# Kernel optimization log

Hardware: AMD Instinct MI355X
Metric: run time of the kernel (lower is better)

## Reference

```python
import jax, jax.numpy as jnp
import numpy as np

B = 8192
N_CLASSES = 10

_AX = 'abcd'
_CNOT = jnp.array([[1, 0, 0, 0], [0, 1, 0, 0], [0, 0, 0, 1], [0, 0, 1, 0]], jnp.float32).reshape(2, 2, 2, 2)


def _ry(theta):
    c, s = jnp.cos(theta / 2), jnp.sin(theta / 2)
    return jnp.stack([jnp.stack([c, -s]), jnp.stack([s, c])])  # [2,2]


def _ap1(state, U, w):
    # apply single-qubit gate U on wire w; state: [N,2,2,2,2]
    i = _AX[:w] + 'i' + _AX[w + 1:]
    o = _AX[:w] + 'o' + _AX[w + 1:]
    return jnp.einsum(f'oi,n{i}->n{o}', U, state)


def _ap2(state, U, w0, w1):
    # apply two-qubit gate U [2,2,2,2]=(out0,out1,in0,in1) on wires (w0,w1)
    i, o = list(_AX), list(_AX)
    i[w0], i[w1] = 'i', 'j'
    o[w0], o[w1] = 'o', 'p'
    return jnp.einsum(f"opij,n{''.join(i)}->n{''.join(o)}", U, state)


def quantum_features(data, q_params):
    # data: [N,4] RY encoding angles applied to |0000>
    h = data / 2
    v = jnp.stack([jnp.cos(h), jnp.sin(h)], -1)  # [N,4,2]
    state = jnp.einsum('na,nb,nc,nd->nabcd', v[:, 0], v[:, 1], v[:, 2], v[:, 3])
    # fixed 8-op random layer instance (real-valued): 5 RY + 3 CNOT
    state = _ap1(state, _ry(q_params[0]), 0)
    state = _ap1(state, _ry(q_params[1]), 1)
    state = _ap2(state, _CNOT, 0, 1)
    state = _ap1(state, _ry(q_params[2]), 2)
    state = _ap1(state, _ry(q_params[3]), 3)
    state = _ap2(state, _CNOT, 2, 3)
    state = _ap1(state, _ry(q_params[4]), 1)
    state = _ap2(state, _CNOT, 1, 2)
    probs = state * state  # real statevector -> |amp|^2
    sgn = jnp.array([1.0, -1.0], jnp.float32)
    z = jnp.stack([
        jnp.einsum('nabcd,a->n', probs, sgn),
        jnp.einsum('nabcd,b->n', probs, sgn),
        jnp.einsum('nabcd,c->n', probs, sgn),
        jnp.einsum('nabcd,d->n', probs, sgn)], -1)
    return z  # [N,4] PauliZ expectations


def setup_inputs() -> dict:
    key = jax.random.key(0)
    ks = jax.random.split(key, 6)
    return {
        'x': jax.random.normal(ks[0], (B, 1, 28, 28), jnp.float32),
        'conv_w': jax.random.normal(ks[1], (4, 1, 2, 2), jnp.float32) * 0.5,
        'conv_b': jax.random.normal(ks[2], (4,), jnp.float32) * 0.1,
        'q_params': jax.random.uniform(ks[3], (5,), jnp.float32, 0.0, 2.0 * np.pi),
        'lin_w': jax.random.normal(ks[4], (N_CLASSES, 1568), jnp.float32) * 0.02,
        'lin_b': jnp.zeros((N_CLASSES,), jnp.float32),
    }


def reference(x, conv_w, conv_b, q_params, lin_w, lin_b):
    feats = jax.lax.conv_general_dilated(
        x, conv_w, window_strides=(2, 2), padding='VALID',
        dimension_numbers=('NCHW', 'OIHW', 'NCHW')) + conv_b[None, :, None, None]
    bsz = feats.shape[0]
    flat = feats.reshape(bsz, -1)  # [B,784]
    # extractor views flat as [B,28,28] and takes 2x2 patches -> [B*196,4]
    patches = flat.reshape(bsz, 14, 2, 14, 2).transpose(0, 1, 3, 2, 4).reshape(bsz * 196, 4)
    q = quantum_features(patches, q_params).reshape(bsz, 784)
    combined = jnp.concatenate([flat, q], axis=1)  # [B,1568]
    logits = combined @ lin_w.T + lin_b
    return jax.nn.log_softmax(logits, axis=-1)
```

## Files before the change

### kernel.cpp

```cpp
#include <hip/hip_runtime.h>
#include <hip/hip_bf16.h>


#define SPB 8
#define THREADS 256
#define NCLS 10
#define FEAT 1568

__global__ __launch_bounds__(THREADS, 3)
void quanv_fused_kernel(const float* __restrict__ x,
                        const float* __restrict__ conv_w,
                        const float* __restrict__ conv_b,
                        const float* __restrict__ q_params,
                        const float* __restrict__ lin_w,
                        const float* __restrict__ lin_b,
                        float* __restrict__ out)
{
    __shared__ float comb[SPB][FEAT];

    const int tid = threadIdx.x;
    const int n0  = blockIdx.x * SPB;

    float W[4][4], Bc[4];
    #pragma unroll
    for (int c = 0; c < 4; ++c) {
        #pragma unroll
        for (int k = 0; k < 4; ++k) W[c][k] = conv_w[c * 4 + k];
        Bc[c] = conv_b[c];
    }
    const float qp0 = q_params[0], qp1 = q_params[1];
    const float qp2 = q_params[2], qp3 = q_params[3];
    const float q4  = q_params[4];
    const float cq4 = cosf(q4), sq4 = sinf(q4);

    for (int p = tid; p < SPB * 196; p += THREADS) {
        const int s = p / 196, r = p % 196;
        const int h = r / 14, w = r % 14;
        const float* xp = x + (size_t)(n0 + s) * 784 + (2 * h) * 28 + 2 * w;
        const float x00 = xp[0], x01 = xp[1], x10 = xp[28], x11 = xp[29];
        #pragma unroll
        for (int c = 0; c < 4; ++c) {
            comb[s][c * 196 + r] =
                fmaf(x00, W[c][0], fmaf(x01, W[c][1],
                fmaf(x10, W[c][2], fmaf(x11, W[c][3], Bc[c]))));
        }
    }
    __syncthreads();

    for (int p = tid; p < SPB * 196; p += THREADS) {
        const int s = p / 196, r = p % 196;
        const int i = r / 14, j = r % 14;
        const int base = 56 * i + 2 * j;
        const float d0 = comb[s][base],      d1 = comb[s][base + 1];
        const float d2 = comb[s][base + 28], d3 = comb[s][base + 29];
        const float a0 = d0 + qp0, a1 = d1 + qp1;
        const float a2 = d2 + qp2, a3 = d3 + qp3;
        const float c0 = cosf(a0);
        const float c1 = cosf(a1), s1 = sinf(a1);
        const float c2 = cosf(a2), c3 = cosf(a3);
        const float z0 = c0;
        const float z1 = cq4 * c0 * c1 - sq4 * s1;
        const float z2 = z1 * c2;
        const float z3 = c2 * c3;
        *reinterpret_cast<float4*>(&comb[s][784 + r * 4]) =
            make_float4(z0, z1, z2, z3);
    }
    __syncthreads();

    const int wave = tid >> 6, lane = tid & 63;
    const int s0 = 2 * wave, s1 = s0 + 1;

    float acc0[NCLS], acc1[NCLS];
    #pragma unroll
    for (int c = 0; c < NCLS; ++c) { acc0[c] = 0.f; acc1[c] = 0.f; }

    for (int k = lane; k < FEAT; k += 64) {
        const float v0 = comb[s0][k];
        const float v1 = comb[s1][k];
        #pragma unroll
        for (int c = 0; c < NCLS; ++c) {
            const float lw = lin_w[c * FEAT + k];
            acc0[c] = fmaf(v0, lw, acc0[c]);
            acc1[c] = fmaf(v1, lw, acc1[c]);
        }
    }

    #pragma unroll
    for (int m = 1; m < 64; m <<= 1) {
        #pragma unroll
        for (int c = 0; c < NCLS; ++c) {
            acc0[c] += __shfl_xor(acc0[c], m, 64);
            acc1[c] += __shfl_xor(acc1[c], m, 64);
        }
    }

    if (lane == 0) {
        float lg[NCLS], mx = -1e30f;
        #pragma unroll
        for (int c = 0; c < NCLS; ++c) {
            lg[c] = acc0[c] + lin_b[c];
            mx = fmaxf(mx, lg[c]);
        }
        float sum = 0.f;
        #pragma unroll
        for (int c = 0; c < NCLS; ++c) sum += expf(lg[c] - mx);
        const float lse = mx + logf(sum);
        float* o = out + (size_t)(n0 + s0) * NCLS;
        #pragma unroll
        for (int c = 0; c < NCLS; ++c) o[c] = lg[c] - lse;
    } else if (lane == 1) {
        float lg[NCLS], mx = -1e30f;
        #pragma unroll
        for (int c = 0; c < NCLS; ++c) {
            lg[c] = acc1[c] + lin_b[c];
            mx = fmaxf(mx, lg[c]);
        }
        float sum = 0.f;
        #pragma unroll
        for (int c = 0; c < NCLS; ++c) sum += expf(lg[c] - mx);
        const float lse = mx + logf(sum);
        float* o = out + (size_t)(n0 + s1) * NCLS;
        #pragma unroll
        for (int c = 0; c < NCLS; ++c) o[c] = lg[c] - lse;
    }
}

extern "C" void kernel_launch(void* const* d_in, const int* in_sizes, int n_in,
                              void* d_out, int out_size, void* d_ws, size_t ws_size,
                              hipStream_t stream) {
    const float* x        = (const float*)d_in[0];
    const float* conv_w   = (const float*)d_in[1];
    const float* conv_b   = (const float*)d_in[2];
    const float* q_params = (const float*)d_in[3];
    const float* lin_w    = (const float*)d_in[4];
    const float* lin_b    = (const float*)d_in[5];
    float* out = (float*)d_out;

    const int B = in_sizes[0] / 784;
    const int nblocks = B / SPB;

    quanv_fused_kernel<<<nblocks, THREADS, 0, stream>>>(
        x, conv_w, conv_b, q_params, lin_w, lin_b, out);
}
```

Measured before the change: 107.4 us.

## Halve samples per block, vectorize loads, and use fast intrinsics

Measured after the change: 103.0 us. -4.1%, faster.

```diff
diff --git a/kernel.cpp b/kernel.cpp
--- a/kernel.cpp
+++ b/kernel.cpp
@@ -2,12 +2,12 @@
 #include <hip/hip_bf16.h>
 
 
-#define SPB 8
+#define SPB 4
 #define THREADS 256
 #define NCLS 10
 #define FEAT 1568
 
-__global__ __launch_bounds__(THREADS, 3)
+__global__ __launch_bounds__(THREADS, 6)
 void quanv_fused_kernel(const float* __restrict__ x,
                         const float* __restrict__ conv_w,
                         const float* __restrict__ conv_b,
@@ -31,18 +31,23 @@
     const float qp0 = q_params[0], qp1 = q_params[1];
     const float qp2 = q_params[2], qp3 = q_params[3];
     const float q4  = q_params[4];
-    const float cq4 = cosf(q4), sq4 = sinf(q4);
+    const float cq4 = __cosf(q4), sq4 = __sinf(q4);
 
-    for (int p = tid; p < SPB * 196; p += THREADS) {
-        const int s = p / 196, r = p % 196;
-        const int h = r / 14, w = r % 14;
-        const float* xp = x + (size_t)(n0 + s) * 784 + (2 * h) * 28 + 2 * w;
-        const float x00 = xp[0], x01 = xp[1], x10 = xp[28], x11 = xp[29];
+    for (int p = tid; p < SPB * 14 * 7; p += THREADS) {
+        const int s = p / 98, t = p % 98;
+        const int h = t / 7, wp = t % 7;
+        const float* xp = x + (size_t)(n0 + s) * 784 + 56 * h + 4 * wp;
+        const float4 r0 = *reinterpret_cast<const float4*>(xp);
+        const float4 r1 = *reinterpret_cast<const float4*>(xp + 28);
+        const int r = h * 14 + 2 * wp;
         #pragma unroll
         for (int c = 0; c < 4; ++c) {
             comb[s][c * 196 + r] =
-                fmaf(x00, W[c][0], fmaf(x01, W[c][1],
-                fmaf(x10, W[c][2], fmaf(x11, W[c][3], Bc[c]))));
+                fmaf(r0.x, W[c][0], fmaf(r0.y, W[c][1],
+                fmaf(r1.x, W[c][2], fmaf(r1.y, W[c][3], Bc[c]))));
+            comb[s][c * 196 + r + 1] =
+                fmaf(r0.z, W[c][0], fmaf(r0.w, W[c][1],
+                fmaf(r1.z, W[c][2], fmaf(r1.w, W[c][3], Bc[c]))));
         }
     }
     __syncthreads();
@@ -51,13 +56,13 @@
         const int s = p / 196, r = p % 196;
         const int i = r / 14, j = r % 14;
         const int base = 56 * i + 2 * j;
-        const float d0 = comb[s][base],      d1 = comb[s][base + 1];
-        const float d2 = comb[s][base + 28], d3 = comb[s][base + 29];
-        const float a0 = d0 + qp0, a1 = d1 + qp1;
-        const float a2 = d2 + qp2, a3 = d3 + qp3;
-        const float c0 = cosf(a0);
-        const float c1 = cosf(a1), s1 = sinf(a1);
-        const float c2 = cosf(a2), c3 = cosf(a3);
+        const float2 d01 = *reinterpret_cast<const float2*>(&comb[s][base]);
+        const float2 d23 = *reinterpret_cast<const float2*>(&comb[s][base + 28]);
+        const float a0 = d01.x + qp0, a1 = d01.y + qp1;
+        const float a2 = d23.x + qp2, a3 = d23.y + qp3;
+        const float c0 = __cosf(a0);
+        const float c1 = __cosf(a1), s1 = __sinf(a1);
+        const float c2 = __cosf(a2), c3 = __cosf(a3);
         const float z0 = c0;
         const float z1 = cq4 * c0 * c1 - sq4 * s1;
         const float z2 = z1 * c2;
@@ -68,58 +73,50 @@
     __syncthreads();
 
     const int wave = tid >> 6, lane = tid & 63;
-    const int s0 = 2 * wave, s1 = s0 + 1;
+    const int s = wave;
 
-    float acc0[NCLS], acc1[NCLS];
+    float acc[NCLS];
     #pragma unroll
-    for (int c = 0; c < NCLS; ++c) { acc0[c] = 0.f; acc1[c] = 0.f; }
+    for (int c = 0; c < NCLS; ++c) acc[c] = 0.f;
 
-    for (int k = lane; k < FEAT; k += 64) {
-        const float v0 = comb[s0][k];
-        const float v1 = comb[s1][k];
+    #pragma unroll
+    for (int kb = 0; kb < 6; ++kb) {
+        const int k = kb * 256 + lane * 4;
+        const float4 v = *reinterpret_cast<const float4*>(&comb[s][k]);
         #pragma unroll
         for (int c = 0; c < NCLS; ++c) {
-            const float lw = lin_w[c * FEAT + k];
-            acc0[c] = fmaf(v0, lw, acc0[c]);
-            acc1[c] = fmaf(v1, lw, acc1[c]);
+            const float4 w4 = *reinterpret_cast<const float4*>(&lin_w[c * FEAT + k]);
+            acc[c] = fmaf(v.x, w4.x, fmaf(v.y, w4.y,
+                     fmaf(v.z, w4.z, fmaf(v.w, w4.w, acc[c]))));
         }
+    }
+    if (lane < 32) {
+        const int k = 1536 + lane;
+        const float v = comb[s][k];
+        #pragma unroll
+        for (int c = 0; c < NCLS; ++c)
+            acc[c] = fmaf(v, lin_w[c * FEAT + k], acc[c]);
     }
 
     #pragma unroll
     for (int m = 1; m < 64; m <<= 1) {
         #pragma unroll
-        for (int c = 0; c < NCLS; ++c) {
-            acc0[c] += __shfl_xor(acc0[c], m, 64);
-            acc1[c] += __shfl_xor(acc1[c], m, 64);
-        }
+        for (int c = 0; c < NCLS; ++c)
+            acc[c] += __shfl_xor(acc[c], m, 64);
     }
 
     if (lane == 0) {
         float lg[NCLS], mx = -1e30f;
         #pragma unroll
         for (int c = 0; c < NCLS; ++c) {
-            lg[c] = acc0[c] + lin_b[c];
+            lg[c] = acc[c] + lin_b[c];
             mx = fmaxf(mx, lg[c]);
         }
         float sum = 0.f;
         #pragma unroll
-        for (int c = 0; c < NCLS; ++c) sum += expf(lg[c] - mx);
-        const float lse = mx + logf(sum);
-        float* o = out + (size_t)(n0 + s0) * NCLS;
-        #pragma unroll
-        for (int c = 0; c < NCLS; ++c) o[c] = lg[c] - lse;
-    } else if (lane == 1) {
-        float lg[NCLS], mx = -1e30f;
-        #pragma unroll
-        for (int c = 0; c < NCLS; ++c) {
-            lg[c] = acc1[c] + lin_b[c];
-            mx = fmaxf(mx, lg[c]);
-        }
-        float sum = 0.f;
-        #pragma unroll
-        for (int c = 0; c < NCLS; ++c) sum += expf(lg[c] - mx);
-        const float lse = mx + logf(sum);
-        float* o = out + (size_t)(n0 + s1) * NCLS;
+        for (int c = 0; c < NCLS; ++c) sum += __expf(lg[c] - mx);
+        const float lse = mx + __logf(sum);
+        float* o = out + (size_t)(n0 + s) * NCLS;
         #pragma unroll
         for (int c = 0; c < NCLS; ++c) o[c] = lg[c] - lse;
     }
```
